# Performance work log

Hardware: AMD Instinct MI355X
Metric: run time of the kernel (lower is better)

The kernel has to match this reference:

```python
import jax, jax.numpy as jnp
import numpy as np

B, T, I = 8, 128, 196
TEXT_DIM, IMAGE_DIM, HIDDEN = 768, 1024, 512


def setup_inputs() -> dict:
    key = jax.random.key(0)
    ks = jax.random.split(key, 7)
    s = lambda d: 1.0 / np.sqrt(d)
    return {
        "text_features": jax.random.normal(ks[0], (B, T, TEXT_DIM), jnp.float32),
        "image_features": jax.random.normal(ks[1], (B, I, IMAGE_DIM), jnp.float32),
        "Wt": jax.random.normal(ks[2], (TEXT_DIM, HIDDEN), jnp.float32) * s(TEXT_DIM),
        "bt": jax.random.normal(ks[3], (HIDDEN,), jnp.float32) * s(TEXT_DIM),
        "Wi": jax.random.normal(ks[4], (IMAGE_DIM, HIDDEN), jnp.float32) * s(IMAGE_DIM),
        "bi": jax.random.normal(ks[5], (HIDDEN,), jnp.float32) * s(IMAGE_DIM),
        "wa": jax.random.normal(ks[6], (HIDDEN,), jnp.float32) * s(HIDDEN),
        "ba": jnp.zeros((1,), jnp.float32),
    }


def reference(text_features, image_features, Wt, bt, Wi, bi, wa, ba):
    # projections: [B,T,H] and [B,I,H]
    pt = jnp.einsum("btd,dh->bth", text_features, Wt) + bt
    pi = jnp.einsum("bid,dh->bih", image_features, Wi) + bi
    # additive Bahdanau scores: tanh of broadcast sum [B,T,I,H], reduced by wa
    h = jnp.tanh(pt[:, :, None, :] + pi[:, None, :, :])
    scores = jnp.einsum("btih,h->bti", h, wa) + ba[0]  # [B,T,I]
    text_attended = jnp.einsum("bti,bid->btd", jax.nn.softmax(scores, axis=-1), image_features)
    image_attended = jnp.einsum("bti,btd->bid", jax.nn.softmax(scores, axis=1), text_features)
    return text_attended, image_attended
```

## Files before the change

kernel.cpp:

```cpp
#include <hip/hip_runtime.h>
#include <math.h>

#define B 8
#define T 128
#define I_TOK 196
#define TEXT_DIM 768
#define IMAGE_DIM 1024
#define HIDDEN 512
#define EXP_SCALE 2.88539008177792681f

#if __has_builtin(__builtin_amdgcn_exp2f)
#define FAST_EXP2(x) __builtin_amdgcn_exp2f(x)
#else
#define FAST_EXP2(x) exp2f(x)
#endif
#if __has_builtin(__builtin_amdgcn_rcpf)
#define FAST_RCP(x) __builtin_amdgcn_rcpf(x)
#else
#define FAST_RCP(x) __fdividef(1.f, (x))
#endif
#if __has_builtin(__builtin_amdgcn_sched_barrier)
#define SCHED_FENCE() __builtin_amdgcn_sched_barrier(0)
#else
#define SCHED_FENCE()
#endif

typedef short bf16x8 __attribute__((ext_vector_type(8)));
typedef float f32x4 __attribute__((ext_vector_type(4)));

#define KT_T (TEXT_DIM / 32)
#define KT_I (IMAGE_DIM / 32)
#define MT_T (B * T / 16)
#define MT_I (B * I_TOK / 16)
#define NT   (HIDDEN / 16)

#define XT_ELEMS (MT_T * KT_T * 512)
#define XI_ELEMS (MT_I * KT_I * 512)
#define X_ELEMS  (XT_ELEMS + XI_ELEMS)
#define WT_T_ELEMS (NT * KT_T * 512)
#define W_ELEMS (WT_T_ELEMS + NT * KT_I * 512)

#define XTILES_T (MT_T * KT_T)
#define XTILES   (XTILES_T + MT_I * KT_I)
#define WTILES_T (NT * KT_T)
#define WTILES   (WTILES_T + NT * KT_I)
#define PREP_GRID ((XTILES + WTILES) / 4)

__device__ __forceinline__ unsigned short f2bf(float x) {
    unsigned int u = __float_as_uint(x);
    unsigned int r = u + 0x7FFFu + ((u >> 16) & 1u);
    return (unsigned short)(r >> 16);
}
__device__ __forceinline__ float bf2f(unsigned short h) {
    return __uint_as_float(((unsigned int)h) << 16);
}

__global__ __launch_bounds__(256) void prep_kernel(
        const float* __restrict__ text, const float* __restrict__ image,
        const float* __restrict__ Wt, const float* __restrict__ Wi,
        unsigned short* __restrict__ Xh, unsigned short* __restrict__ Xl,
        unsigned short* __restrict__ WTh, unsigned short* __restrict__ WTl)
{
    const int tid = threadIdx.x;
    const int lane = tid & 63, wv = tid >> 6;
    const int r16 = lane & 15, quad = lane >> 4;
    const int id = blockIdx.x * 4 + wv;

    float v[8];
    unsigned short* oh;
    unsigned short* ol;
    long dst;

    if (id < XTILES) {
        const float* X; int K, mt, kt;
        if (id < XTILES_T) { X = text; K = TEXT_DIM; mt = id / KT_T; kt = id % KT_T; }
        else { const int i2 = id - XTILES_T; X = image; K = IMAGE_DIM; mt = i2 / KT_I; kt = i2 % KT_I; }
        const float* src = X + (long)(mt * 16 + r16) * K + kt * 32 + quad * 8;
        const float4 a = *(const float4*)src;
        const float4 b = *(const float4*)(src + 4);
        v[0]=a.x; v[1]=a.y; v[2]=a.z; v[3]=a.w; v[4]=b.x; v[5]=b.y; v[6]=b.z; v[7]=b.w;
        oh = (id < XTILES_T) ? Xh : Xh + XT_ELEMS;
        ol = (id < XTILES_T) ? Xl : Xl + XT_ELEMS;
        const long tile = (id < XTILES_T) ? id : (long)(id - XTILES_T);
        dst = tile * 512 + lane * 8;
    } else {
        const int idw = id - XTILES;
        const float* W; int K, nt, kt;
        if (idw < WTILES_T) { W = Wt; K = TEXT_DIM; nt = idw / KT_T; kt = idw % KT_T; }
        else { const int i2 = idw - WTILES_T; W = Wi; K = IMAGE_DIM; nt = i2 / KT_I; kt = i2 % KT_I; }
        const float* src = W + (long)(kt * 32 + quad * 8) * HIDDEN + nt * 16 + r16;
        #pragma unroll
        for (int j = 0; j < 8; ++j) v[j] = src[(long)j * HIDDEN];
        oh = (idw < WTILES_T) ? WTh : WTh + WT_T_ELEMS;
        ol = (idw < WTILES_T) ? WTl : WTl + WT_T_ELEMS;
        const long tile = (idw < WTILES_T) ? idw : (long)(idw - WTILES_T);
        dst = tile * 512 + lane * 8;
    }

    uint4 hv, lv;
    unsigned int hh[8], ll[8];
    #pragma unroll
    for (int j = 0; j < 8; ++j) {
        hh[j] = f2bf(v[j]);
        ll[j] = f2bf(v[j] - bf2f((unsigned short)hh[j]));
    }
    hv.x = hh[0] | (hh[1] << 16); hv.y = hh[2] | (hh[3] << 16);
    hv.z = hh[4] | (hh[5] << 16); hv.w = hh[6] | (hh[7] << 16);
    lv.x = ll[0] | (ll[1] << 16); lv.y = ll[2] | (ll[3] << 16);
    lv.z = ll[4] | (ll[5] << 16); lv.w = ll[6] | (ll[7] << 16);
    *(uint4*)(oh + dst) = hv;
    *(uint4*)(ol + dst) = lv;
}

#define GT_BLOCKS (32 * 8)
#define GI_BLOCKS (49 * 8)
#define GEMM_GRID (GT_BLOCKS + GI_BLOCKS)
#define PSTRIDE 66

__global__ __launch_bounds__(256, 2) void mfma_proj_kernel(
        const unsigned short* __restrict__ Xh, const unsigned short* __restrict__ Xl,
        const unsigned short* __restrict__ WTh, const unsigned short* __restrict__ WTl,
        const float* __restrict__ bt, const float* __restrict__ bi,
        float* __restrict__ pt, float* __restrict__ pi)
{
    __shared__ float part[32 * PSTRIDE];

    const int tid = threadIdx.x;
    const int lane = tid & 63, wv = tid >> 6;
    const int r16 = lane & 15, quad = lane >> 4;
    const int nh = wv & 1;
    const int kh = wv >> 1;

    int bid = blockIdx.x;
    const unsigned short *xh, *xl, *wh, *wl; const float* bias; float* Y;
    int ktiles;
    if (bid < GT_BLOCKS) {
        xh = Xh; xl = Xl; wh = WTh; wl = WTl; bias = bt; Y = pt; ktiles = KT_T;
    } else {
        bid -= GT_BLOCKS;
        xh = Xh + XT_ELEMS; xl = Xl + XT_ELEMS;
        wh = WTh + WT_T_ELEMS; wl = WTl + WT_T_ELEMS;
        bias = bi; Y = pi; ktiles = KT_I;
    }
    const int m0 = (bid >> 3) * 32;
    const int n0 = (bid & 7) * 64 + nh * 32;
    const int nstep = ktiles >> 1;
    const int kt0 = kh * nstep;
    const int mt0 = (bid >> 3) * 2;
    const int nt0 = (bid & 7) * 4 + nh * 2;

    const unsigned short* pa0 = xh + ((long)mt0 * ktiles + kt0) * 512 + lane * 8;
    const unsigned short* pa1 = pa0 + (long)ktiles * 512;
    const unsigned short* qa0 = xl + ((long)mt0 * ktiles + kt0) * 512 + lane * 8;
    const unsigned short* qa1 = qa0 + (long)ktiles * 512;
    const unsigned short* pb0 = wh + ((long)nt0 * ktiles + kt0) * 512 + lane * 8;
    const unsigned short* pb1 = pb0 + (long)ktiles * 512;
    const unsigned short* qb0 = wl + ((long)nt0 * ktiles + kt0) * 512 + lane * 8;
    const unsigned short* qb1 = qb0 + (long)ktiles * 512;

    f32x4 a00 = {0,0,0,0}, a01 = {0,0,0,0}, a10 = {0,0,0,0}, a11 = {0,0,0,0};

    bf16x8 Ah0 = *(const bf16x8*)(pa0);
    bf16x8 Ah1 = *(const bf16x8*)(pa1);
    bf16x8 Al0 = *(const bf16x8*)(qa0);
    bf16x8 Al1 = *(const bf16x8*)(qa1);
    bf16x8 Bh0 = *(const bf16x8*)(pb0);
    bf16x8 Bh1 = *(const bf16x8*)(pb1);
    bf16x8 Bl0 = *(const bf16x8*)(qb0);
    bf16x8 Bl1 = *(const bf16x8*)(qb1);

    for (int s = 0; s < nstep; ++s) {
        const long kn = (s + 1 < nstep) ? (long)(s + 1) * 512 : 0;
        const bf16x8 nAh0 = *(const bf16x8*)(pa0 + kn);
        const bf16x8 nAh1 = *(const bf16x8*)(pa1 + kn);
        const bf16x8 nAl0 = *(const bf16x8*)(qa0 + kn);
        const bf16x8 nAl1 = *(const bf16x8*)(qa1 + kn);
        const bf16x8 nBh0 = *(const bf16x8*)(pb0 + kn);
        const bf16x8 nBh1 = *(const bf16x8*)(pb1 + kn);
        const bf16x8 nBl0 = *(const bf16x8*)(qb0 + kn);
        const bf16x8 nBl1 = *(const bf16x8*)(qb1 + kn);
        SCHED_FENCE();

        a00 = __builtin_amdgcn_mfma_f32_16x16x32_bf16(Ah0, Bh0, a00, 0, 0, 0);
        a01 = __builtin_amdgcn_mfma_f32_16x16x32_bf16(Ah0, Bh1, a01, 0, 0, 0);
        a10 = __builtin_amdgcn_mfma_f32_16x16x32_bf16(Ah1, Bh0, a10, 0, 0, 0);
        a11 = __builtin_amdgcn_mfma_f32_16x16x32_bf16(Ah1, Bh1, a11, 0, 0, 0);
        a00 = __builtin_amdgcn_mfma_f32_16x16x32_bf16(Ah0, Bl0, a00, 0, 0, 0);
        a01 = __builtin_amdgcn_mfma_f32_16x16x32_bf16(Ah0, Bl1, a01, 0, 0, 0);
        a10 = __builtin_amdgcn_mfma_f32_16x16x32_bf16(Ah1, Bl0, a10, 0, 0, 0);
        a11 = __builtin_amdgcn_mfma_f32_16x16x32_bf16(Ah1, Bl1, a11, 0, 0, 0);
        a00 = __builtin_amdgcn_mfma_f32_16x16x32_bf16(Al0, Bh0, a00, 0, 0, 0);
        a01 = __builtin_amdgcn_mfma_f32_16x16x32_bf16(Al0, Bh1, a01, 0, 0, 0);
        a10 = __builtin_amdgcn_mfma_f32_16x16x32_bf16(Al1, Bh0, a10, 0, 0, 0);
        a11 = __builtin_amdgcn_mfma_f32_16x16x32_bf16(Al1, Bh1, a11, 0, 0, 0);
        SCHED_FENCE();

        Ah0 = nAh0; Ah1 = nAh1; Al0 = nAl0; Al1 = nAl1;
        Bh0 = nBh0; Bh1 = nBh1; Bl0 = nBl0; Bl1 = nBl1;
    }

    const int lc = nh * 32 + r16;
    if (kh == 1) {
        #pragma unroll
        for (int r = 0; r < 4; ++r) {
            part[(quad * 4 + r) * PSTRIDE + lc]           = a00[r];
            part[(quad * 4 + r) * PSTRIDE + lc + 16]      = a01[r];
            part[(quad * 4 + 16 + r) * PSTRIDE + lc]      = a10[r];
            part[(quad * 4 + 16 + r) * PSTRIDE + lc + 16] = a11[r];
        }
    }
    __syncthreads();
    if (kh == 0) {
        const int row0 = m0 + quad * 4;
        const float bv0 = bias[n0 + r16];
        const float bv1 = bias[n0 + 16 + r16];
        #pragma unroll
        for (int r = 0; r < 4; ++r) {
            const float v00 = (a00[r] + part[(quad * 4 + r) * PSTRIDE + lc]           + bv0) * EXP_SCALE;
            const float v01 = (a01[r] + part[(quad * 4 + r) * PSTRIDE + lc + 16]      + bv1) * EXP_SCALE;
            const float v10 = (a10[r] + part[(quad * 4 + 16 + r) * PSTRIDE + lc]      + bv0) * EXP_SCALE;
            const float v11 = (a11[r] + part[(quad * 4 + 16 + r) * PSTRIDE + lc + 16] + bv1) * EXP_SCALE;
            Y[(long)(row0 + r)      * HIDDEN + n0 + r16]      = FAST_EXP2(v00);
            Y[(long)(row0 + r)      * HIDDEN + n0 + 16 + r16] = FAST_EXP2(v01);
            Y[(long)(row0 + 16 + r) * HIDDEN + n0 + r16]      = FAST_EXP2(v10);
            Y[(long)(row0 + 16 + r) * HIDDEN + n0 + 16 + r16] = FAST_EXP2(v11);
        }
    }
}

__global__ __launch_bounds__(256, 8) void scores_kernel(const float* __restrict__ pt,
        const float* __restrict__ pi, const float* __restrict__ wa,
        const float* __restrict__ ba, float* __restrict__ scores)
{
    const int blk = blockIdx.x;
    const int bt = blk >> 1;
    const int half = blk & 1;
    const int b = bt >> 7;
    const int tid = threadIdx.x;
    const int lane = tid & 63, wave = tid >> 6;

    const float* ptrow = pt + (long)bt * HIDDEN + lane * 8;
    const float4 pA = *(const float4*)ptrow;
    const float4 pB = *(const float4*)(ptrow + 4);
    float4 wA = *(const float4*)(wa + lane * 8);
    float4 wB = *(const float4*)(wa + lane * 8 + 4);

    float S = wA.x + wA.y + wA.z + wA.w + wB.x + wB.y + wB.z + wB.w;
    #pragma unroll
    for (int off = 32; off; off >>= 1) S += __shfl_down(S, off);
    const float base = S + ba[0];

    wA.x *= -2.f; wA.y *= -2.f; wA.z *= -2.f; wA.w *= -2.f;
    wB.x *= -2.f; wB.y *= -2.f; wB.z *= -2.f; wB.w *= -2.f;

    const float* pib = pi + (long)b * I_TOK * HIDDEN + lane * 8;
    const int i0 = half * 98 + wave;
    const int iend = half * 98 + 98;

    float4 ca = *(const float4*)(pib + (long)i0 * HIDDEN);
    float4 cb = *(const float4*)(pib + (long)i0 * HIDDEN + 4);

    for (int i = i0; i < iend; i += 4) {
        const int inx = (i + 4 < iend) ? (i + 4) : i;
        const float4 na = *(const float4*)(pib + (long)inx * HIDDEN);
        const float4 nb = *(const float4*)(pib + (long)inx * HIDDEN + 4);

        float acc = 0.f;
        acc = fmaf(wA.x, FAST_RCP(fmaf(pA.x, ca.x, 1.f)), acc);
        acc = fmaf(wA.y, FAST_RCP(fmaf(pA.y, ca.y, 1.f)), acc);
        acc = fmaf(wA.z, FAST_RCP(fmaf(pA.z, ca.z, 1.f)), acc);
        acc = fmaf(wA.w, FAST_RCP(fmaf(pA.w, ca.w, 1.f)), acc);
        acc = fmaf(wB.x, FAST_RCP(fmaf(pB.x, cb.x, 1.f)), acc);
        acc = fmaf(wB.y, FAST_RCP(fmaf(pB.y, cb.y, 1.f)), acc);
        acc = fmaf(wB.z, FAST_RCP(fmaf(pB.z, cb.z, 1.f)), acc);
        acc = fmaf(wB.w, FAST_RCP(fmaf(pB.w, cb.w, 1.f)), acc);

        #pragma unroll
        for (int off = 32; off; off >>= 1) acc += __shfl_down(acc, off);
        if (lane == 0) scores[(long)bt * I_TOK + i] = base + acc;
        ca = na; cb = nb;
    }
}

__global__ __launch_bounds__(256) void att_kernel(const float* __restrict__ scores,
        const float* __restrict__ image, const float* __restrict__ text,
        float* __restrict__ out_text, float* __restrict__ out_img)
{
    const int tid = threadIdx.x, lane = tid & 63, wave = tid >> 6;

    if (blockIdx.x < 512) {
        const int bid = blockIdx.x;
        const int csplit = bid & 1;
        const int grp = bid >> 1;
        const int b = grp >> 5;
        const int t0 = (grp & 31) * 4;

        __shared__ float ps[I_TOK][4];
        {
            const float* srow = scores + ((long)(b * T + t0 + wave)) * I_TOK;
            const float s0 = srow[lane];
            const float s1 = srow[lane + 64];
            const float s2 = srow[lane + 128];
            const float s3 = (lane < 4) ? srow[lane + 192] : -INFINITY;
            float m = fmaxf(fmaxf(s0, s1), fmaxf(s2, s3));
            #pragma unroll
            for (int off = 32; off; off >>= 1) m = fmaxf(m, __shfl_xor(m, off));
            const float e0 = __expf(s0 - m);
            const float e1 = __expf(s1 - m);
            const float e2 = __expf(s2 - m);
            const float e3 = (lane < 4) ? __expf(s3 - m) : 0.f;
            float sum = e0 + e1 + e2 + e3;
            #pragma unroll
            for (int off = 32; off; off >>= 1) sum += __shfl_xor(sum, off);
            const float inv = __fdividef(1.0f, sum);
            ps[lane][wave] = e0 * inv;
            ps[lane + 64][wave] = e1 * inv;
            ps[lane + 128][wave] = e2 * inv;
            if (lane < 4) ps[lane + 192][wave] = e3 * inv;
        }
        __syncthreads();

        const float* img = image + (long)b * I_TOK * IMAGE_DIM + csplit * 512 + tid * 2;
        float a00 = 0.f, a01 = 0.f, a10 = 0.f, a11 = 0.f;
        float a20 = 0.f, a21 = 0.f, a30 = 0.f, a31 = 0.f;

        float2 v0 = *(const float2*)(img + 0 * IMAGE_DIM);
        float2 v1 = *(const float2*)(img + 1 * IMAGE_DIM);
        float2 v2 = *(const float2*)(img + 2 * IMAGE_DIM);
        float2 v3 = *(const float2*)(img + 3 * IMAGE_DIM);
        float4 p0 = *(const float4*)&ps[0][0];
        float4 p1 = *(const float4*)&ps[1][0];
        float4 p2 = *(const float4*)&ps[2][0];
        float4 p3 = *(const float4*)&ps[3][0];

        for (int g = 0; g < 49; ++g) {
            const int ib = (g + 1 < 49) ? (g + 1) * 4 : g * 4;
            const float2 w0 = *(const float2*)(img + (long)(ib + 0) * IMAGE_DIM);
            const float2 w1 = *(const float2*)(img + (long)(ib + 1) * IMAGE_DIM);
            const float2 w2 = *(const float2*)(img + (long)(ib + 2) * IMAGE_DIM);
            const float2 w3 = *(const float2*)(img + (long)(ib + 3) * IMAGE_DIM);
            const float4 r0 = *(const float4*)&ps[ib + 0][0];
            const float4 r1 = *(const float4*)&ps[ib + 1][0];
            const float4 r2 = *(const float4*)&ps[ib + 2][0];
            const float4 r3 = *(const float4*)&ps[ib + 3][0];
            a00 = fmaf(p0.x, v0.x, a00); a01 = fmaf(p0.x, v0.y, a01);
            a10 = fmaf(p0.y, v0.x, a10); a11 = fmaf(p0.y, v0.y, a11);
            a20 = fmaf(p0.z, v0.x, a20); a21 = fmaf(p0.z, v0.y, a21);
            a30 = fmaf(p0.w, v0.x, a30); a31 = fmaf(p0.w, v0.y, a31);
            a00 = fmaf(p1.x, v1.x, a00); a01 = fmaf(p1.x, v1.y, a01);
            a10 = fmaf(p1.y, v1.x, a10); a11 = fmaf(p1.y, v1.y, a11);
            a20 = fmaf(p1.z, v1.x, a20); a21 = fmaf(p1.z, v1.y, a21);
            a30 = fmaf(p1.w, v1.x, a30); a31 = fmaf(p1.w, v1.y, a31);
            a00 = fmaf(p2.x, v2.x, a00); a01 = fmaf(p2.x, v2.y, a01);
            a10 = fmaf(p2.y, v2.x, a10); a11 = fmaf(p2.y, v2.y, a11);
            a20 = fmaf(p2.z, v2.x, a20); a21 = fmaf(p2.z, v2.y, a21);
            a30 = fmaf(p2.w, v2.x, a30); a31 = fmaf(p2.w, v2.y, a31);
            a00 = fmaf(p3.x, v3.x, a00); a01 = fmaf(p3.x, v3.y, a01);
            a10 = fmaf(p3.y, v3.x, a10); a11 = fmaf(p3.y, v3.y, a11);
            a20 = fmaf(p3.z, v3.x, a20); a21 = fmaf(p3.z, v3.y, a21);
            a30 = fmaf(p3.w, v3.x, a30); a31 = fmaf(p3.w, v3.y, a31);
            v0 = w0; v1 = w1; v2 = w2; v3 = w3;
            p0 = r0; p1 = r1; p2 = r2; p3 = r3;
        }
        float* o = out_text + ((long)(b * T + t0)) * IMAGE_DIM + csplit * 512 + tid * 2;
        float2 w;
        w.x = a00; w.y = a01; *(float2*)(o + 0 * IMAGE_DIM) = w;
        w.x = a10; w.y = a11; *(float2*)(o + 1 * IMAGE_DIM) = w;
        w.x = a20; w.y = a21; *(float2*)(o + 2 * IMAGE_DIM) = w;
        w.x = a30; w.y = a31; *(float2*)(o + 3 * IMAGE_DIM) = w;
    } else {
        const int bid = blockIdx.x - 512;
        const int b = bid / (I_TOK / 4);
        const int i0 = (bid % (I_TOK / 4)) * 4;

        __shared__ float qs[T][4];
        {
            const float* sc = scores + (long)b * T * I_TOK + (i0 + wave);
            const float s0 = sc[(long)lane * I_TOK];
            const float s1 = sc[(long)(lane + 64) * I_TOK];
            float m = fmaxf(s0, s1);
            #pragma unroll
            for (int off = 32; off; off >>= 1) m = fmaxf(m, __shfl_xor(m, off));
            const float e0 = __expf(s0 - m);
            const float e1 = __expf(s1 - m);
            float sum = e0 + e1;
            #pragma unroll
            for (int off = 32; off; off >>= 1) sum += __shfl_xor(sum, off);
            const float inv = __fdividef(1.0f, sum);
            qs[lane][wave] = e0 * inv;
            qs[lane + 64][wave] = e1 * inv;
        }
        __syncthreads();

        const float* txt2 = text + (long)b * T * TEXT_DIM + tid * 2;
        const float* txt1 = text + (long)b * T * TEXT_DIM + 512 + tid;
        float a00=0.f,a01=0.f,a02=0.f, a10=0.f,a11=0.f,a12=0.f;
        float a20=0.f,a21=0.f,a22=0.f, a30=0.f,a31=0.f,a32=0.f;

        float2 u0 = *(const float2*)(txt2 + 0 * TEXT_DIM);
        float2 u1 = *(const float2*)(txt2 + 1 * TEXT_DIM);
        float  z0 = txt1[0 * TEXT_DIM];
        float  z1 = txt1[1 * TEXT_DIM];
        float4 q0 = *(const float4*)&qs[0][0];
        float4 q1 = *(const float4*)&qs[1][0];

        for (int g = 0; g < 64; ++g) {
            const int tb = (g + 1 < 64) ? (g + 1) * 2 : g * 2;
            const float2 nu0 = *(const float2*)(txt2 + (long)(tb + 0) * TEXT_DIM);
            const float2 nu1 = *(const float2*)(txt2 + (long)(tb + 1) * TEXT_DIM);
            const float  nz0 = txt1[(long)(tb + 0) * TEXT_DIM];
            const float  nz1 = txt1[(long)(tb + 1) * TEXT_DIM];
            const float4 nq0 = *(const float4*)&qs[tb + 0][0];
            const float4 nq1 = *(const float4*)&qs[tb + 1][0];
            a00 = fmaf(q0.x, u0.x, a00); a01 = fmaf(q0.x, u0.y, a01); a02 = fmaf(q0.x, z0, a02);
            a10 = fmaf(q0.y, u0.x, a10); a11 = fmaf(q0.y, u0.y, a11); a12 = fmaf(q0.y, z0, a12);
            a20 = fmaf(q0.z, u0.x, a20); a21 = fmaf(q0.z, u0.y, a21); a22 = fmaf(q0.z, z0, a22);
            a30 = fmaf(q0.w, u0.x, a30); a31 = fmaf(q0.w, u0.y, a31); a32 = fmaf(q0.w, z0, a32);
            a00 = fmaf(q1.x, u1.x, a00); a01 = fmaf(q1.x, u1.y, a01); a02 = fmaf(q1.x, z1, a02);
            a10 = fmaf(q1.y, u1.x, a10); a11 = fmaf(q1.y, u1.y, a11); a12 = fmaf(q1.y, z1, a12);
            a20 = fmaf(q1.z, u1.x, a20); a21 = fmaf(q1.z, u1.y, a21); a22 = fmaf(q1.z, z1, a22);
            a30 = fmaf(q1.w, u1.x, a30); a31 = fmaf(q1.w, u1.y, a31); a32 = fmaf(q1.w, z1, a32);
            u0 = nu0; u1 = nu1; z0 = nz0; z1 = nz1; q0 = nq0; q1 = nq1;
        }
        float* o = out_img + ((long)b * I_TOK + i0) * TEXT_DIM;
        float2 w;
        w.x = a00; w.y = a01; *(float2*)(o + 0 * TEXT_DIM + tid * 2) = w; o[0 * TEXT_DIM + 512 + tid] = a02;
        w.x = a10; w.y = a11; *(float2*)(o + 1 * TEXT_DIM + tid * 2) = w; o[1 * TEXT_DIM + 512 + tid] = a12;
        w.x = a20; w.y = a21; *(float2*)(o + 2 * TEXT_DIM + tid * 2) = w; o[2 * TEXT_DIM + 512 + tid] = a22;
        w.x = a30; w.y = a31; *(float2*)(o + 3 * TEXT_DIM + tid * 2) = w; o[3 * TEXT_DIM + 512 + tid] = a32;
    }
}

extern "C" void kernel_launch(void* const* d_in, const int* in_sizes, int n_in,
                              void* d_out, int out_size, void* d_ws, size_t ws_size,
                              hipStream_t stream) {
    const float* text  = (const float*)d_in[0];
    const float* image = (const float*)d_in[1];
    const float* Wt    = (const float*)d_in[2];
    const float* bt    = (const float*)d_in[3];
    const float* Wi    = (const float*)d_in[4];
    const float* bi    = (const float*)d_in[5];
    const float* wa    = (const float*)d_in[6];
    const float* ba    = (const float*)d_in[7];

    float* pt = (float*)d_ws;
    float* pi = pt + (long)B * T * HIDDEN;
    float* sc = pi + (long)B * I_TOK * HIDDEN;
    unsigned short* Xh  = (unsigned short*)(sc + (long)B * T * I_TOK);
    unsigned short* Xl  = Xh + X_ELEMS;
    unsigned short* WTh = Xl + X_ELEMS;
    unsigned short* WTl = WTh + W_ELEMS;

    float* out_text = (float*)d_out;
    float* out_img  = out_text + (long)B * T * IMAGE_DIM;

    prep_kernel<<<PREP_GRID, 256, 0, stream>>>(text, image, Wt, Wi, Xh, Xl, WTh, WTl);
    mfma_proj_kernel<<<GEMM_GRID, 256, 0, stream>>>(Xh, Xl, WTh, WTl, bt, bi, pt, pi);
    scores_kernel<<<2 * B * T, 256, 0, stream>>>(pt, pi, wa, ba, sc);
    att_kernel<<<512 + B * (I_TOK / 4), 256, 0, stream>>>(sc, image, text, out_text, out_img);
}
```

Measured before the change: 144.9 us.

## Transpose image projection layout and restructure scores kernel to thread-per-image-token

The projection GEMM now stores the exponentiated image projection transposed per batch as [H][I], so the scores kernel can assign one thread per image token and loop over hidden, reusing each loaded image value for two text rows. This removes the per-score cross-lane shuffle reduction and folds the -2 scale into a final FMA. The trade-offs are scattered strided stores in the GEMM epilogue, only 512 blocks with 196 of 256 threads active, and serial per-thread loops over 512 hidden elements.

```diff
diff --git a/kernel.cpp b/kernel.cpp
--- a/kernel.cpp
+++ b/kernel.cpp
@@ -116,12 +116,13 @@
 #define GI_BLOCKS (49 * 8)
 #define GEMM_GRID (GT_BLOCKS + GI_BLOCKS)
 #define PSTRIDE 66
+#define EIT_B (HIDDEN * I_TOK)
 
 __global__ __launch_bounds__(256, 2) void mfma_proj_kernel(
         const unsigned short* __restrict__ Xh, const unsigned short* __restrict__ Xl,
         const unsigned short* __restrict__ WTh, const unsigned short* __restrict__ WTl,
         const float* __restrict__ bt, const float* __restrict__ bi,
-        float* __restrict__ pt, float* __restrict__ pi)
+        float* __restrict__ pt, float* __restrict__ EiT)
 {
     __shared__ float part[32 * PSTRIDE];
 
@@ -132,15 +133,15 @@
     const int kh = wv >> 1;
 
     int bid = blockIdx.x;
-    const unsigned short *xh, *xl, *wh, *wl; const float* bias; float* Y;
-    int ktiles;
+    const unsigned short *xh, *xl, *wh, *wl; const float* bias;
+    int ktiles, is_text;
     if (bid < GT_BLOCKS) {
-        xh = Xh; xl = Xl; wh = WTh; wl = WTl; bias = bt; Y = pt; ktiles = KT_T;
+        xh = Xh; xl = Xl; wh = WTh; wl = WTl; bias = bt; ktiles = KT_T; is_text = 1;
     } else {
         bid -= GT_BLOCKS;
         xh = Xh + XT_ELEMS; xl = Xl + XT_ELEMS;
         wh = WTh + WT_T_ELEMS; wl = WTl + WT_T_ELEMS;
-        bias = bi; Y = pi; ktiles = KT_I;
+        bias = bi; ktiles = KT_I; is_text = 0;
     }
     const int m0 = (bid >> 3) * 32;
     const int n0 = (bid & 7) * 64 + nh * 32;
@@ -211,74 +212,72 @@
     }
     __syncthreads();
     if (kh == 0) {
-        const int row0 = m0 + quad * 4;
         const float bv0 = bias[n0 + r16];
         const float bv1 = bias[n0 + 16 + r16];
+        const int h0 = n0 + r16, h1 = n0 + 16 + r16;
         #pragma unroll
         for (int r = 0; r < 4; ++r) {
-            const float v00 = (a00[r] + part[(quad * 4 + r) * PSTRIDE + lc]           + bv0) * EXP_SCALE;
-            const float v01 = (a01[r] + part[(quad * 4 + r) * PSTRIDE + lc + 16]      + bv1) * EXP_SCALE;
-            const float v10 = (a10[r] + part[(quad * 4 + 16 + r) * PSTRIDE + lc]      + bv0) * EXP_SCALE;
-            const float v11 = (a11[r] + part[(quad * 4 + 16 + r) * PSTRIDE + lc + 16] + bv1) * EXP_SCALE;
-            Y[(long)(row0 + r)      * HIDDEN + n0 + r16]      = FAST_EXP2(v00);
-            Y[(long)(row0 + r)      * HIDDEN + n0 + 16 + r16] = FAST_EXP2(v01);
-            Y[(long)(row0 + 16 + r) * HIDDEN + n0 + r16]      = FAST_EXP2(v10);
-            Y[(long)(row0 + 16 + r) * HIDDEN + n0 + 16 + r16] = FAST_EXP2(v11);
-        }
-    }
-}
-
-__global__ __launch_bounds__(256, 8) void scores_kernel(const float* __restrict__ pt,
-        const float* __restrict__ pi, const float* __restrict__ wa,
+            const float v00 = FAST_EXP2((a00[r] + part[(quad * 4 + r) * PSTRIDE + lc]           + bv0) * EXP_SCALE);
+            const float v01 = FAST_EXP2((a01[r] + part[(quad * 4 + r) * PSTRIDE + lc + 16]      + bv1) * EXP_SCALE);
+            const float v10 = FAST_EXP2((a10[r] + part[(quad * 4 + 16 + r) * PSTRIDE + lc]      + bv0) * EXP_SCALE);
+            const float v11 = FAST_EXP2((a11[r] + part[(quad * 4 + 16 + r) * PSTRIDE + lc + 16] + bv1) * EXP_SCALE);
+            const int row0 = m0 + quad * 4 + r;
+            const int row1 = row0 + 16;
+            if (is_text) {
+                pt[(long)row0 * HIDDEN + h0] = v00;
+                pt[(long)row0 * HIDDEN + h1] = v01;
+                pt[(long)row1 * HIDDEN + h0] = v10;
+                pt[(long)row1 * HIDDEN + h1] = v11;
+            } else {
+                const int b0 = row0 / I_TOK, i0 = row0 - b0 * I_TOK;
+                const int b1 = row1 / I_TOK, i1 = row1 - b1 * I_TOK;
+                EiT[(long)b0 * EIT_B + (long)h0 * I_TOK + i0] = v00;
+                EiT[(long)b0 * EIT_B + (long)h1 * I_TOK + i0] = v01;
+                EiT[(long)b1 * EIT_B + (long)h0 * I_TOK + i1] = v10;
+                EiT[(long)b1 * EIT_B + (long)h1 * I_TOK + i1] = v11;
+            }
+        }
+    }
+}
+
+__global__ __launch_bounds__(256) void scores_kernel(const float* __restrict__ pt,
+        const float* __restrict__ EiT, const float* __restrict__ wa,
         const float* __restrict__ ba, float* __restrict__ scores)
 {
-    const int blk = blockIdx.x;
-    const int bt = blk >> 1;
-    const int half = blk & 1;
-    const int b = bt >> 7;
+    __shared__ float swa_lds;
     const int tid = threadIdx.x;
-    const int lane = tid & 63, wave = tid >> 6;
-
-    const float* ptrow = pt + (long)bt * HIDDEN + lane * 8;
-    const float4 pA = *(const float4*)ptrow;
-    const float4 pB = *(const float4*)(ptrow + 4);
-    float4 wA = *(const float4*)(wa + lane * 8);
-    float4 wB = *(const float4*)(wa + lane * 8 + 4);
-
-    float S = wA.x + wA.y + wA.z + wA.w + wB.x + wB.y + wB.z + wB.w;
-    #pragma unroll
-    for (int off = 32; off; off >>= 1) S += __shfl_down(S, off);
-    const float base = S + ba[0];
-
-    wA.x *= -2.f; wA.y *= -2.f; wA.z *= -2.f; wA.w *= -2.f;
-    wB.x *= -2.f; wB.y *= -2.f; wB.z *= -2.f; wB.w *= -2.f;
-
-    const float* pib = pi + (long)b * I_TOK * HIDDEN + lane * 8;
-    const int i0 = half * 98 + wave;
-    const int iend = half * 98 + 98;
-
-    float4 ca = *(const float4*)(pib + (long)i0 * HIDDEN);
-    float4 cb = *(const float4*)(pib + (long)i0 * HIDDEN + 4);
-
-    for (int i = i0; i < iend; i += 4) {
-        const int inx = (i + 4 < iend) ? (i + 4) : i;
-        const float4 na = *(const float4*)(pib + (long)inx * HIDDEN);
-        const float4 nb = *(const float4*)(pib + (long)inx * HIDDEN + 4);
-
-        float acc = 0.f;
-        acc = fmaf(wA.x, FAST_RCP(fmaf(pA.x, ca.x, 1.f)), acc);
-        acc = fmaf(wA.y, FAST_RCP(fmaf(pA.y, ca.y, 1.f)), acc);
-        acc = fmaf(wA.z, FAST_RCP(fmaf(pA.z, ca.z, 1.f)), acc);
-        acc = fmaf(wA.w, FAST_RCP(fmaf(pA.w, ca.w, 1.f)), acc);
-        acc = fmaf(wB.x, FAST_RCP(fmaf(pB.x, cb.x, 1.f)), acc);
-        acc = fmaf(wB.y, FAST_RCP(fmaf(pB.y, cb.y, 1.f)), acc);
-        acc = fmaf(wB.z, FAST_RCP(fmaf(pB.z, cb.z, 1.f)), acc);
-        acc = fmaf(wB.w, FAST_RCP(fmaf(pB.w, cb.w, 1.f)), acc);
-
+    const int b = blockIdx.x >> 6;
+    const int t0 = (blockIdx.x & 63) * 2;
+
+    if (tid < 64) {
+        float s = 0.f;
         #pragma unroll
-        for (int off = 32; off; off >>= 1) acc += __shfl_down(acc, off);
-        if (lane == 0) scores[(long)bt * I_TOK + i] = base + acc;
-        ca = na; cb = nb;
+        for (int k = 0; k < 8; ++k) s += wa[tid + k * 64];
+        #pragma unroll
+        for (int off = 32; off; off >>= 1) s += __shfl_xor(s, off);
+        if (tid == 0) swa_lds = s;
+    }
+    __syncthreads();
+    const float base = swa_lds + ba[0];
+
+    const int i = (tid < I_TOK) ? tid : (I_TOK - 1);
+    const float* eib = EiT + (long)b * EIT_B + i;
+    const float* p0 = pt + (long)(b * T + t0) * HIDDEN;
+    const float* p1 = p0 + HIDDEN;
+
+    float acc0 = 0.f, acc1 = 0.f;
+    #pragma unroll 8
+    for (int h = 0; h < HIDDEN; ++h) {
+        const float ei = eib[(long)h * I_TOK];
+        const float w  = wa[h];
+        const float e0 = p0[h];
+        const float e1 = p1[h];
+        acc0 = fmaf(w, FAST_RCP(fmaf(e0, ei, 1.f)), acc0);
+        acc1 = fmaf(w, FAST_RCP(fmaf(e1, ei, 1.f)), acc1);
+    }
+    if (tid < I_TOK) {
+        scores[(long)(b * T + t0)     * I_TOK + tid] = fmaf(-2.f, acc0, base);
+        scores[(long)(b * T + t0 + 1) * I_TOK + tid] = fmaf(-2.f, acc1, base);
     }
 }
 
@@ -443,9 +442,9 @@
     const float* wa    = (const float*)d_in[6];
     const float* ba    = (const float*)d_in[7];
 
-    float* pt = (float*)d_ws;
-    float* pi = pt + (long)B * T * HIDDEN;
-    float* sc = pi + (long)B * I_TOK * HIDDEN;
+    float* pt  = (float*)d_ws;
+    float* EiT = pt + (long)B * T * HIDDEN;
+    float* sc  = EiT + (long)B * EIT_B;
     unsigned short* Xh  = (unsigned short*)(sc + (long)B * T * I_TOK);
     unsigned short* Xl  = Xh + X_ELEMS;
     unsigned short* WTh = Xl + X_ELEMS;
@@ -455,7 +454,7 @@
     float* out_img  = out_text + (long)B * T * IMAGE_DIM;
 
     prep_kernel<<<PREP_GRID, 256, 0, stream>>>(text, image, Wt, Wi, Xh, Xl, WTh, WTl);
-    mfma_proj_kernel<<<GEMM_GRID, 256, 0, stream>>>(Xh, Xl, WTh, WTl, bt, bi, pt, pi);
-    scores_kernel<<<2 * B * T, 256, 0, stream>>>(pt, pi, wa, ba, sc);
+    mfma_proj_kernel<<<GEMM_GRID, 256, 0, stream>>>(Xh, Xl, WTh, WTl, bt, bi, pt, EiT);
+    scores_kernel<<<B * (T / 2), 256, 0, stream>>>(pt, EiT, wa, ba, sc);
     att_kernel<<<512 + B * (I_TOK / 4), 256, 0, stream>>>(sc, image, text, out_text, out_img);
 }
```

After: 153.8 us. +6.1%, slower.
